# Performance work log

Hardware: AMD Instinct MI355X
Metric: run time of the kernel (lower is better)

The kernel has to match this reference:

```python
import jax, jax.numpy as jnp
import numpy as np

EPS = 1e-6


def setup_inputs() -> dict:
    key = jax.random.key(0)
    k1, k2 = jax.random.split(key)
    B, K, N, d = 4, 16, 2048, 256
    return {
        "img_f": jax.random.normal(k1, (B, K, d), dtype=jnp.float32),
        "text_f": jax.random.normal(k2, (N, K, d), dtype=jnp.float32),
        "r": jnp.zeros((4,), dtype=jnp.float32),
        "alp": jnp.array([0.5], dtype=jnp.float32),
        "scale": jnp.array([1.0], dtype=jnp.float32),
        "logits_scales": jnp.array([0.5], dtype=jnp.float32),
    }


def _rc_dist_ItoT(I, T, alpha, beta):
    # I: (B,K,d) images, T: (N,K,d) texts -> dist (B,N)
    B, K, d = I.shape
    lam = (B / d) * jnp.exp(alpha) + EPS
    rho = jnp.exp(beta)
    ItI = jnp.einsum('bkd,bke->bde', I, I)                      # (B,d,d)
    Minv = jnp.linalg.inv(ItI + lam * jnp.eye(d, dtype=I.dtype))
    A = jnp.einsum('bde,bke->bdk', Minv, I)                      # (B,d,K) = Minv @ I^T
    # T_bar[b,n] = I[b] @ A[b] @ T[n]; fuse P = I @ A (B,K,K) to avoid (B,N,d,d) W.
    P = jnp.einsum('bkd,bdj->bkj', I, A)                         # (B,K,K)
    T_bar = jnp.einsum('bkj,njd->bnkd', P, T) * rho              # (B,N,K,d)
    diff = T_bar - T[None]
    return -jnp.sum(diff * diff, axis=-1).mean(axis=-1)          # (B,N)


def _rc_dist_TtoI(I, T, alpha, beta):
    # per-text ridge projector applied to images -> dist (B,N)
    N, K, d = T.shape
    lam = (N / d) * jnp.exp(alpha) + EPS
    rho = jnp.exp(beta)
    TtT = jnp.einsum('nkd,nke->nde', T, T)                       # (N,d,d)
    Minv = jnp.linalg.inv(TtT + lam * jnp.eye(d, dtype=T.dtype))
    A = jnp.einsum('nde,nke->ndk', Minv, T)                      # (N,d,K)
    Q = jnp.einsum('nkd,ndj->nkj', T, A)                         # (N,K,K)
    I_bar = jnp.einsum('nkj,bjd->nbkd', Q, I) * rho              # (N,B,K,d)
    diff = I_bar - I[None]
    return (-jnp.sum(diff * diff, axis=-1).mean(axis=-1)).T      # (B,N)


def reference(img_f, text_f, r, alp, scale, logits_scales):
    d1 = _rc_dist_ItoT(img_f, text_f, r[0], r[1])
    d2 = _rc_dist_TtoI(img_f, text_f, r[2], r[3])
    rc_dist = alp * d1 + (1.0 - alp) * d2
    logits = rc_dist * scale
    logits_pre = jax.nn.log_softmax(logits, axis=1)
    return logits_pre, jax.nn.sigmoid(logits_scales)
```

## Files before the change

kernel.cpp:

```cpp
#include <hip/hip_runtime.h>
#include <math.h>

#define Bq 4
#define Kq 16
#define Nq 2048
#define Dq 256

typedef float f32x4 __attribute__((ext_vector_type(4)));
typedef short s16x8 __attribute__((ext_vector_type(8)));


static __device__ __forceinline__ unsigned short f2bf(float x) {
    union { float f; unsigned u; } v; v.f = x;
    unsigned r = v.u + 0x7fff + ((v.u >> 16) & 1);
    return (unsigned short)(r >> 16);
}
static __device__ __forceinline__ float bf2f(unsigned short b) {
    union { float f; unsigned u; } v; v.u = ((unsigned)b) << 16;
    return v.f;
}

__device__ __forceinline__ void solve_wave(const float* __restrict__ Xp,
                                           float lam, float rho,
                                           float (*Aug)[34], int lane,
                                           f32x4* g_out, f32x4* s_out) {
    const int arow = lane & 15;
    const int kgrp = lane >> 4;

    float x[64];
    const float* base = Xp + arow * Dq + kgrp * 8;
#pragma unroll
    for (int c = 0; c < 8; ++c) {
        const float4 a = *reinterpret_cast<const float4*>(base + c * 32);
        const float4 b = *reinterpret_cast<const float4*>(base + c * 32 + 4);
        x[c * 8 + 0] = a.x; x[c * 8 + 1] = a.y; x[c * 8 + 2] = a.z; x[c * 8 + 3] = a.w;
        x[c * 8 + 4] = b.x; x[c * 8 + 5] = b.y; x[c * 8 + 6] = b.z; x[c * 8 + 7] = b.w;
    }

    f32x4 g = {0.f, 0.f, 0.f, 0.f};
#pragma unroll
    for (int c = 0; c < 8; ++c) {
        s16x8 h, lo;
#pragma unroll
        for (int e = 0; e < 8; ++e) {
            const float xv = x[c * 8 + e];
            const unsigned short hb = f2bf(xv);
            h[e]  = (short)hb;
            lo[e] = (short)f2bf(xv - bf2f(hb));
        }
        g = __builtin_amdgcn_mfma_f32_16x16x32_bf16(h, h, g, 0, 0, 0);
        g = __builtin_amdgcn_mfma_f32_16x16x32_bf16(h, lo, g, 0, 0, 0);
        g = __builtin_amdgcn_mfma_f32_16x16x32_bf16(lo, h, g, 0, 0, 0);
    }

    const int ccol = lane & 15;
#pragma unroll
    for (int q = 0; q < 4; ++q) {
        const int rr = kgrp * 4 + q;
        const float gg = g[q];
        const float dv = (rr == ccol) ? lam : 0.f;
        float2 pr; pr.x = gg + dv; pr.y = (rho - 1.f) * gg - dv;
        *reinterpret_cast<float2*>(&Aug[rr][2 * ccol]) = pr;
    }
    __builtin_amdgcn_wave_barrier();

    for (int k = 0; k < Kq; ++k) {
        const float2 pv = *reinterpret_cast<const float2*>(&Aug[k][2 * k]);
        const float pinv = 1.0f / pv.x;
        const float2 pk = *reinterpret_cast<const float2*>(&Aug[k][2 * ccol]);
        float fac[4];
#pragma unroll
        for (int q = 0; q < 4; ++q) fac[q] = Aug[kgrp * 4 + q][2 * k];
        __builtin_amdgcn_wave_barrier();
#pragma unroll
        for (int q = 0; q < 4; ++q) {
            const int rr = kgrp * 4 + q;
            float2 cur = *reinterpret_cast<const float2*>(&Aug[rr][2 * ccol]);
            const float f = fac[q] * pinv;
            float2 nw;
            nw.x = (rr == k) ? pk.x * pinv : cur.x - f * pk.x;
            nw.y = (rr == k) ? pk.y * pinv : cur.y - f * pk.y;
            *reinterpret_cast<float2*>(&Aug[rr][2 * ccol]) = nw;
        }
        __builtin_amdgcn_wave_barrier();
    }

    s16x8 mh, ml;
#pragma unroll
    for (int e = 0; e < 8; ++e) {
        const int kk = (kgrp & 1) * 8 + e;
        const float mv = (lane < 32) ? Aug[arow][2 * kk + 1] : 0.f;
        const unsigned short hb = f2bf(mv);
        mh[e] = (short)hb;
        ml[e] = (short)f2bf(mv - bf2f(hb));
    }
    f32x4 s = {0.f, 0.f, 0.f, 0.f};
    s = __builtin_amdgcn_mfma_f32_16x16x32_bf16(mh, mh, s, 0, 0, 0);
    s = __builtin_amdgcn_mfma_f32_16x16x32_bf16(mh, ml, s, 0, 0, 0);
    s = __builtin_amdgcn_mfma_f32_16x16x32_bf16(ml, mh, s, 0, 0, 0);

    *g_out = g;
    *s_out = s;
}

__global__ __launch_bounds__(256) void phase1_kernel(const float* __restrict__ img,
                                                     const float* __restrict__ r,
                                                     float* __restrict__ ws) {
    __shared__ __align__(16) float Aug[4][Kq][34];
    const int tid = threadIdx.x;
    const int w = tid >> 6, lane = tid & 63;
    const float lam = (float(Bq) / float(Dq)) * expf(r[0]) + 1e-6f;
    const float rho = expf(r[1]);
    f32x4 g, s;
    solve_wave(img + w * (Kq * Dq), lam, rho, Aug[w], lane, &g, &s);
    reinterpret_cast<f32x4*>(ws)[w * 64 + lane] = s;
    reinterpret_cast<f32x4*>(ws + 1024)[w * 64 + lane] = g;
}

__global__ __launch_bounds__(64) void phase2_kernel(const float* __restrict__ text,
                                                    const float* __restrict__ r,
                                                    const float* __restrict__ alp,
                                                    const float* __restrict__ scale,
                                                    const float* __restrict__ sg,
                                                    float* __restrict__ logits) {
    __shared__ __align__(16) float Aug[Kq][34];
    const int n = blockIdx.x;
    const int lane = threadIdx.x;
    const float lam = (float(Nq) / float(Dq)) * expf(r[2]) + 1e-6f;
    const float rho = expf(r[3]);
    f32x4 g, s;
    solve_wave(text + n * (Kq * Dq), lam, rho, Aug, lane, &g, &s);

    float p[8];
#pragma unroll
    for (int b = 0; b < 4; ++b) {
        const f32x4 s1 = reinterpret_cast<const f32x4*>(sg)[b * 64 + lane];
        const f32x4 gi = reinterpret_cast<const f32x4*>(sg + 1024)[b * 64 + lane];
        p[b]     = s1.x * g.x + s1.y * g.y + s1.z * g.z + s1.w * g.w;
        p[4 + b] = gi.x * s.x + gi.y * s.y + gi.z * s.z + gi.w * s.w;
    }
#pragma unroll
    for (int off = 32; off; off >>= 1) {
#pragma unroll
        for (int q = 0; q < 8; ++q) p[q] += __shfl_down(p[q], off, 64);
    }
    if (lane == 0) {
        const float a = alp[0], sc = scale[0];
#pragma unroll
        for (int b = 0; b < 4; ++b) {
            const float d1 = -p[b] * (1.f / Kq);
            const float d2 = -p[4 + b] * (1.f / Kq);
            logits[b * Nq + n] = sc * (a * d1 + (1.f - a) * d2);
        }
    }
}

__global__ __launch_bounds__(256) void phase3_kernel(const float* __restrict__ logits,
                                                     const float* __restrict__ lsc,
                                                     float* __restrict__ out) {
    const int b   = blockIdx.x;
    const int tid = threadIdx.x;
    const float* row = logits + b * Nq;
    __shared__ float sh[4];
    float v[8];
    float mx = -INFINITY;
#pragma unroll
    for (int q = 0; q < 8; ++q) {
        v[q] = row[tid + q * 256];
        mx = fmaxf(mx, v[q]);
    }
#pragma unroll
    for (int off = 32; off; off >>= 1) mx = fmaxf(mx, __shfl_down(mx, off, 64));
    if ((tid & 63) == 0) sh[tid >> 6] = mx;
    __syncthreads();
    mx = fmaxf(fmaxf(sh[0], sh[1]), fmaxf(sh[2], sh[3]));

    float sum = 0.f;
#pragma unroll
    for (int q = 0; q < 8; ++q) sum += expf(v[q] - mx);
#pragma unroll
    for (int off = 32; off; off >>= 1) sum += __shfl_down(sum, off, 64);
    __syncthreads();
    if ((tid & 63) == 0) sh[tid >> 6] = sum;
    __syncthreads();
    sum = sh[0] + sh[1] + sh[2] + sh[3];

    const float lse = mx + logf(sum);
#pragma unroll
    for (int q = 0; q < 8; ++q) out[b * Nq + tid + q * 256] = v[q] - lse;
    if (b == 0 && tid == 0) out[Bq * Nq] = 1.f / (1.f + expf(-lsc[0]));
}

extern "C" void kernel_launch(void* const* d_in, const int* in_sizes, int n_in,
                              void* d_out, int out_size, void* d_ws, size_t ws_size,
                              hipStream_t stream) {
    const float* img   = (const float*)d_in[0];
    const float* text  = (const float*)d_in[1];
    const float* r     = (const float*)d_in[2];
    const float* alp   = (const float*)d_in[3];
    const float* scale = (const float*)d_in[4];
    const float* lsc   = (const float*)d_in[5];
    float* ws  = (float*)d_ws;
    float* out = (float*)d_out;

    phase1_kernel<<<1, 256, 0, stream>>>(img, r, ws);
    phase2_kernel<<<Nq, 64, 0, stream>>>(text, r, alp, scale, ws, ws + 2048);
    phase3_kernel<<<Bq, 256, 0, stream>>>(ws + 2048, lsc, out);
}
```

Before: 25.03 us.

## Fuse image solve into per-text kernel and use hardware bf16 pack conversion

Removes the single-block phase1 kernel. Every block of the text kernel now redundantly recomputes the small image Gram matrix and its 16x16 solve, and shares the results through shared memory, which drops one launch and a serialized dependency. Blocks grow to four waves, one text item per wave. The manual bf16 rounding is replaced with the v_cvt_pk_bf16_f32 instruction. The cost is redundant image work in all 512 blocks, more registers, and more shared memory per block.

```diff
diff --git a/kernel.cpp b/kernel.cpp
--- a/kernel.cpp
+++ b/kernel.cpp
@@ -8,136 +8,151 @@
 
 typedef float f32x4 __attribute__((ext_vector_type(4)));
 typedef short s16x8 __attribute__((ext_vector_type(8)));
-
-
-static __device__ __forceinline__ unsigned short f2bf(float x) {
-    union { float f; unsigned u; } v; v.f = x;
-    unsigned r = v.u + 0x7fff + ((v.u >> 16) & 1);
-    return (unsigned short)(r >> 16);
-}
-static __device__ __forceinline__ float bf2f(unsigned short b) {
-    union { float f; unsigned u; } v; v.u = ((unsigned)b) << 16;
-    return v.f;
-}
-
-__device__ __forceinline__ void solve_wave(const float* __restrict__ Xp,
-                                           float lam, float rho,
-                                           float (*Aug)[34], int lane,
-                                           f32x4* g_out, f32x4* s_out) {
-    const int arow = lane & 15;
-    const int kgrp = lane >> 4;
-
-    float x[64];
-    const float* base = Xp + arow * Dq + kgrp * 8;
-#pragma unroll
-    for (int c = 0; c < 8; ++c) {
-        const float4 a = *reinterpret_cast<const float4*>(base + c * 32);
-        const float4 b = *reinterpret_cast<const float4*>(base + c * 32 + 4);
-        x[c * 8 + 0] = a.x; x[c * 8 + 1] = a.y; x[c * 8 + 2] = a.z; x[c * 8 + 3] = a.w;
-        x[c * 8 + 4] = b.x; x[c * 8 + 5] = b.y; x[c * 8 + 6] = b.z; x[c * 8 + 7] = b.w;
-    }
-
-    f32x4 g = {0.f, 0.f, 0.f, 0.f};
-#pragma unroll
-    for (int c = 0; c < 8; ++c) {
-        s16x8 h, lo;
-#pragma unroll
-        for (int e = 0; e < 8; ++e) {
-            const float xv = x[c * 8 + e];
-            const unsigned short hb = f2bf(xv);
-            h[e]  = (short)hb;
-            lo[e] = (short)f2bf(xv - bf2f(hb));
-        }
-        g = __builtin_amdgcn_mfma_f32_16x16x32_bf16(h, h, g, 0, 0, 0);
-        g = __builtin_amdgcn_mfma_f32_16x16x32_bf16(h, lo, g, 0, 0, 0);
-        g = __builtin_amdgcn_mfma_f32_16x16x32_bf16(lo, h, g, 0, 0, 0);
-    }
-
-    const int ccol = lane & 15;
-#pragma unroll
-    for (int q = 0; q < 4; ++q) {
-        const int rr = kgrp * 4 + q;
-        const float gg = g[q];
-        const float dv = (rr == ccol) ? lam : 0.f;
-        float2 pr; pr.x = gg + dv; pr.y = (rho - 1.f) * gg - dv;
-        *reinterpret_cast<float2*>(&Aug[rr][2 * ccol]) = pr;
-    }
-    __builtin_amdgcn_wave_barrier();
-
-    for (int k = 0; k < Kq; ++k) {
-        const float2 pv = *reinterpret_cast<const float2*>(&Aug[k][2 * k]);
-        const float pinv = 1.0f / pv.x;
-        const float2 pk = *reinterpret_cast<const float2*>(&Aug[k][2 * ccol]);
-        float fac[4];
-#pragma unroll
-        for (int q = 0; q < 4; ++q) fac[q] = Aug[kgrp * 4 + q][2 * k];
-        __builtin_amdgcn_wave_barrier();
-#pragma unroll
-        for (int q = 0; q < 4; ++q) {
-            const int rr = kgrp * 4 + q;
-            float2 cur = *reinterpret_cast<const float2*>(&Aug[rr][2 * ccol]);
-            const float f = fac[q] * pinv;
-            float2 nw;
-            nw.x = (rr == k) ? pk.x * pinv : cur.x - f * pk.x;
-            nw.y = (rr == k) ? pk.y * pinv : cur.y - f * pk.y;
-            *reinterpret_cast<float2*>(&Aug[rr][2 * ccol]) = nw;
-        }
-        __builtin_amdgcn_wave_barrier();
-    }
-
-    s16x8 mh, ml;
-#pragma unroll
-    for (int e = 0; e < 8; ++e) {
-        const int kk = (kgrp & 1) * 8 + e;
-        const float mv = (lane < 32) ? Aug[arow][2 * kk + 1] : 0.f;
-        const unsigned short hb = f2bf(mv);
-        mh[e] = (short)hb;
-        ml[e] = (short)f2bf(mv - bf2f(hb));
-    }
-    f32x4 s = {0.f, 0.f, 0.f, 0.f};
-    s = __builtin_amdgcn_mfma_f32_16x16x32_bf16(mh, mh, s, 0, 0, 0);
-    s = __builtin_amdgcn_mfma_f32_16x16x32_bf16(mh, ml, s, 0, 0, 0);
-    s = __builtin_amdgcn_mfma_f32_16x16x32_bf16(ml, mh, s, 0, 0, 0);
-
-    *g_out = g;
-    *s_out = s;
-}
-
-__global__ __launch_bounds__(256) void phase1_kernel(const float* __restrict__ img,
-                                                     const float* __restrict__ r,
-                                                     float* __restrict__ ws) {
-    __shared__ __align__(16) float Aug[4][Kq][34];
-    const int tid = threadIdx.x;
-    const int w = tid >> 6, lane = tid & 63;
-    const float lam = (float(Bq) / float(Dq)) * expf(r[0]) + 1e-6f;
-    const float rho = expf(r[1]);
-    f32x4 g, s;
-    solve_wave(img + w * (Kq * Dq), lam, rho, Aug[w], lane, &g, &s);
-    reinterpret_cast<f32x4*>(ws)[w * 64 + lane] = s;
-    reinterpret_cast<f32x4*>(ws + 1024)[w * 64 + lane] = g;
-}
-
-__global__ __launch_bounds__(64) void phase2_kernel(const float* __restrict__ text,
+typedef unsigned int u32;
+
+union frag_u { s16x8 v; u32 w[4]; };
+
+static __device__ __forceinline__ u32 cvtpk(float a, float b) {
+    u32 r;
+    asm("v_cvt_pk_bf16_f32 %0, %1, %2" : "=v"(r) : "v"(a), "v"(b));
+    return r;
+}
+
+static __device__ __forceinline__ void cvt2(float a, float b, u32* hw, u32* lw) {
+    const u32 h = cvtpk(a, b);
+    const float h0 = __uint_as_float(h << 16);
+    const float h1 = __uint_as_float(h & 0xFFFF0000u);
+    *hw = h;
+    *lw = cvtpk(a - h0, b - h1);
+}
+
+static __device__ __forceinline__ void conv8(const float4 a, const float4 b,
+                                             s16x8* hi, s16x8* lo) {
+    frag_u H, L;
+    cvt2(a.x, a.y, &H.w[0], &L.w[0]);
+    cvt2(a.z, a.w, &H.w[1], &L.w[1]);
+    cvt2(b.x, b.y, &H.w[2], &L.w[2]);
+    cvt2(b.z, b.w, &H.w[3], &L.w[3]);
+    *hi = H.v; *lo = L.v;
+}
+
+#define MFMA(A, B, C) __builtin_amdgcn_mfma_f32_16x16x32_bf16((A), (B), (C), 0, 0, 0)
+
+__global__ __launch_bounds__(256) void fused_kernel(const float* __restrict__ img,
+                                                    const float* __restrict__ text,
                                                     const float* __restrict__ r,
                                                     const float* __restrict__ alp,
                                                     const float* __restrict__ scale,
-                                                    const float* __restrict__ sg,
                                                     float* __restrict__ logits) {
-    __shared__ __align__(16) float Aug[Kq][34];
-    const int n = blockIdx.x;
-    const int lane = threadIdx.x;
-    const float lam = (float(Nq) / float(Dq)) * expf(r[2]) + 1e-6f;
-    const float rho = expf(r[3]);
-    f32x4 g, s;
-    solve_wave(text + n * (Kq * Dq), lam, rho, Aug, lane, &g, &s);
+    __shared__ __align__(16) float AugI[4][Kq][34];
+    __shared__ __align__(16) float AugT[4][Kq][34];
+    __shared__ __align__(16) f32x4 shS1[4][64];
+    __shared__ __align__(16) f32x4 shGI[4][64];
+
+    const int tid  = threadIdx.x;
+    const int w    = tid >> 6, lane = tid & 63;
+    const int arow = lane & 15, kgrp = lane >> 4, ccol = arow;
+    const int n    = blockIdx.x * 4 + w;
+
+    const float lamI = (float(Bq) / float(Dq)) * expf(r[0]) + 1e-6f;
+    const float rhoI = expf(r[1]);
+    const float lamT = (float(Nq) / float(Dq)) * expf(r[2]) + 1e-6f;
+    const float rhoT = expf(r[3]);
+
+    const float* baseI = img  + w * (Kq * Dq) + arow * Dq + kgrp * 8;
+    const float* baseT = text + n * (Kq * Dq) + arow * Dq + kgrp * 8;
+    float4 xi[16], xt[16];
+#pragma unroll
+    for (int c = 0; c < 8; ++c) {
+        xi[2 * c]     = *reinterpret_cast<const float4*>(baseI + c * 32);
+        xi[2 * c + 1] = *reinterpret_cast<const float4*>(baseI + c * 32 + 4);
+        xt[2 * c]     = *reinterpret_cast<const float4*>(baseT + c * 32);
+        xt[2 * c + 1] = *reinterpret_cast<const float4*>(baseT + c * 32 + 4);
+    }
+
+    f32x4 gI = {0.f, 0.f, 0.f, 0.f}, gT = {0.f, 0.f, 0.f, 0.f};
+#pragma unroll
+    for (int c = 0; c < 8; ++c) {
+        s16x8 hi, lo;
+        conv8(xi[2 * c], xi[2 * c + 1], &hi, &lo);
+        gI = MFMA(hi, hi, gI); gI = MFMA(hi, lo, gI); gI = MFMA(lo, hi, gI);
+        conv8(xt[2 * c], xt[2 * c + 1], &hi, &lo);
+        gT = MFMA(hi, hi, gT); gT = MFMA(hi, lo, gT); gT = MFMA(lo, hi, gT);
+    }
+
+    float (*AI)[34] = AugI[w];
+    float (*AT)[34] = AugT[w];
+#pragma unroll
+    for (int q = 0; q < 4; ++q) {
+        const int rr = kgrp * 4 + q;
+        const float dI = (rr == ccol) ? lamI : 0.f;
+        const float dT = (rr == ccol) ? lamT : 0.f;
+        float2 pI; pI.x = gI[q] + dI; pI.y = (rhoI - 1.f) * gI[q] - dI;
+        float2 pT; pT.x = gT[q] + dT; pT.y = (rhoT - 1.f) * gT[q] - dT;
+        *reinterpret_cast<float2*>(&AI[rr][2 * ccol]) = pI;
+        *reinterpret_cast<float2*>(&AT[rr][2 * ccol]) = pT;
+    }
+    __builtin_amdgcn_wave_barrier();
+
+    for (int k = 0; k < Kq; ++k) {
+        const float2 pvI = *reinterpret_cast<const float2*>(&AI[k][2 * k]);
+        const float2 pvT = *reinterpret_cast<const float2*>(&AT[k][2 * k]);
+        const float2 pkI = *reinterpret_cast<const float2*>(&AI[k][2 * ccol]);
+        const float2 pkT = *reinterpret_cast<const float2*>(&AT[k][2 * ccol]);
+        const float piI = 1.f / pvI.x;
+        const float piT = 1.f / pvT.x;
+        float facI[4], facT[4];
+#pragma unroll
+        for (int q = 0; q < 4; ++q) {
+            facI[q] = AI[kgrp * 4 + q][2 * k];
+            facT[q] = AT[kgrp * 4 + q][2 * k];
+        }
+        __builtin_amdgcn_wave_barrier();
+#pragma unroll
+        for (int q = 0; q < 4; ++q) {
+            const int rr = kgrp * 4 + q;
+            float2 cI = *reinterpret_cast<const float2*>(&AI[rr][2 * ccol]);
+            float2 cT = *reinterpret_cast<const float2*>(&AT[rr][2 * ccol]);
+            const float fI = facI[q] * piI;
+            const float fT = facT[q] * piT;
+            float2 nI, nT;
+            nI.x = (rr == k) ? pkI.x * piI : cI.x - fI * pkI.x;
+            nI.y = (rr == k) ? pkI.y * piI : cI.y - fI * pkI.y;
+            nT.x = (rr == k) ? pkT.x * piT : cT.x - fT * pkT.x;
+            nT.y = (rr == k) ? pkT.y * piT : cT.y - fT * pkT.y;
+            *reinterpret_cast<float2*>(&AI[rr][2 * ccol]) = nI;
+            *reinterpret_cast<float2*>(&AT[rr][2 * ccol]) = nT;
+        }
+        __builtin_amdgcn_wave_barrier();
+    }
+
+    frag_u HImg, LImg, HTxt, LTxt;
+#pragma unroll
+    for (int e = 0; e < 8; e += 2) {
+        const int kk = (kgrp & 1) * 8 + e;
+        const bool vld = (lane < 32);
+        const float i0 = vld ? AI[arow][2 * kk + 1]       : 0.f;
+        const float i1 = vld ? AI[arow][2 * (kk + 1) + 1] : 0.f;
+        const float t0 = vld ? AT[arow][2 * kk + 1]       : 0.f;
+        const float t1 = vld ? AT[arow][2 * (kk + 1) + 1] : 0.f;
+        cvt2(i0, i1, &HImg.w[e >> 1], &LImg.w[e >> 1]);
+        cvt2(t0, t1, &HTxt.w[e >> 1], &LTxt.w[e >> 1]);
+    }
+    f32x4 sI = {0.f, 0.f, 0.f, 0.f}, sT = {0.f, 0.f, 0.f, 0.f};
+    sI = MFMA(HImg.v, HImg.v, sI); sI = MFMA(HImg.v, LImg.v, sI); sI = MFMA(LImg.v, HImg.v, sI);
+    sT = MFMA(HTxt.v, HTxt.v, sT); sT = MFMA(HTxt.v, LTxt.v, sT); sT = MFMA(LTxt.v, HTxt.v, sT);
+
+    shS1[w][lane] = sI;
+    shGI[w][lane] = gI;
+    __syncthreads();
 
     float p[8];
 #pragma unroll
     for (int b = 0; b < 4; ++b) {
-        const f32x4 s1 = reinterpret_cast<const f32x4*>(sg)[b * 64 + lane];
-        const f32x4 gi = reinterpret_cast<const f32x4*>(sg + 1024)[b * 64 + lane];
-        p[b]     = s1.x * g.x + s1.y * g.y + s1.z * g.z + s1.w * g.w;
-        p[4 + b] = gi.x * s.x + gi.y * s.y + gi.z * s.z + gi.w * s.w;
+        const f32x4 s1 = shS1[b][lane];
+        const f32x4 gi = shGI[b][lane];
+        p[b]     = s1.x * gT.x + s1.y * gT.y + s1.z * gT.z + s1.w * gT.w;
+        p[4 + b] = gi.x * sT.x + gi.y * sT.y + gi.z * sT.z + gi.w * sT.w;
     }
 #pragma unroll
     for (int off = 32; off; off >>= 1) {
@@ -155,9 +170,9 @@
     }
 }
 
-__global__ __launch_bounds__(256) void phase3_kernel(const float* __restrict__ logits,
-                                                     const float* __restrict__ lsc,
-                                                     float* __restrict__ out) {
+__global__ __launch_bounds__(256) void softmax_kernel(const float* __restrict__ logits,
+                                                      const float* __restrict__ lsc,
+                                                      float* __restrict__ out) {
     const int b   = blockIdx.x;
     const int tid = threadIdx.x;
     const float* row = logits + b * Nq;
@@ -203,7 +218,6 @@
     float* ws  = (float*)d_ws;
     float* out = (float*)d_out;
 
-    phase1_kernel<<<1, 256, 0, stream>>>(img, r, ws);
-    phase2_kernel<<<Nq, 64, 0, stream>>>(text, r, alp, scale, ws, ws + 2048);
-    phase3_kernel<<<Bq, 256, 0, stream>>>(ws + 2048, lsc, out);
-}
+    fused_kernel<<<Nq / 4, 256, 0, stream>>>(img, text, r, alp, scale, ws);
+    softmax_kernel<<<Bq, 256, 0, stream>>>(ws, lsc, out);
+}
```

Result: no change. 24.98 us (-0.2%).
